# Performance work log

Measured on AMD Instinct MI355X. Metric: run time of the kernel, lower is better.

## Reference

```python
import jax, jax.numpy as jnp
import numpy as np
from jax import lax

C = 128       # capacity
D = 64        # latent_dims
K = 512       # K_vecs
BETA = 0.25
DN = ('NCHW', 'OIHW', 'NCHW')


def conv(x, w, b, stride=2, pad=1):
    y = lax.conv_general_dilated(x, w, (stride, stride), ((pad, pad), (pad, pad)),
                                 dimension_numbers=DN)
    return y + b[None, :, None, None]


def conv_transpose(x, w, b, stride=2, pad=1, k=4):
    # PyTorch ConvTranspose2d weight is (Cin, Cout, kh, kw); emulate via
    # lhs-dilated conv with spatially flipped, IO-swapped kernel.
    w2 = jnp.flip(w, axis=(-2, -1)).transpose(1, 0, 2, 3)  # -> OIHW
    p = k - 1 - pad
    y = lax.conv_general_dilated(x, w2, (1, 1), ((p, p), (p, p)),
                                 lhs_dilation=(stride, stride), dimension_numbers=DN)
    return y + b[None, :, None, None]


def setup_inputs() -> dict:
    key = jax.random.key(0)
    ks = jax.random.split(key, 11)
    s = 0.05
    return {
        'x': jax.random.uniform(ks[0], (32, 1, 256, 256), dtype=jnp.float32),
        'enc_w1': jax.random.normal(ks[1], (C, 1, 4, 4), jnp.float32) * s,
        'enc_b1': jnp.zeros((C,), jnp.float32),
        'enc_w2': jax.random.normal(ks[2], (D, C, 4, 4), jnp.float32) * s,
        'enc_b2': jnp.zeros((D,), jnp.float32),
        'codebook': jax.random.normal(ks[3], (K, D), jnp.float32),
        'dec_w2': jax.random.normal(ks[4], (D, C, 4, 4), jnp.float32) * s,  # ConvT: (Cin,Cout,kh,kw)
        'dec_b2': jnp.zeros((C,), jnp.float32),
        'dec_w1': jax.random.normal(ks[5], (C, 1, 4, 4), jnp.float32) * s,
        'dec_b1': jnp.zeros((1,), jnp.float32),
    }


def reference(x, enc_w1, enc_b1, enc_w2, enc_b2, codebook, dec_w2, dec_b2, dec_w1, dec_b1):
    # ---- encoder ----
    h = jax.nn.relu(conv(x, enc_w1, enc_b1))
    z = jax.nn.relu(conv(h, enc_w2, enc_b2))          # [B, D, H/4, W/4]

    # ---- vector quantizer ----
    z_nhwc = jnp.transpose(z, (0, 2, 3, 1))           # [B, h, w, D]
    flat = z_nhwc.reshape(-1, D)                      # [N, D]
    # mean-over-D squared distance, expanded form (no NxKxD tensor)
    d = (jnp.sum(flat * flat, axis=1, keepdims=True)
         - 2.0 * flat @ codebook.T
         + jnp.sum(codebook * codebook, axis=1)[None, :]) / D   # [N, K]
    idx = jnp.argmin(d, axis=1)                       # [N]
    quantized = codebook[idx].reshape(z_nhwc.shape)   # [B, h, w, D]

    codebook_loss = jnp.mean((quantized - lax.stop_gradient(z_nhwc)) ** 2)
    commitment_loss = jnp.mean((lax.stop_gradient(quantized) - z_nhwc) ** 2)
    vq_loss = codebook_loss + BETA * commitment_loss

    # straight-through estimator (training mode)
    quantized_st = z_nhwc + lax.stop_gradient(quantized - z_nhwc)
    q_nchw = jnp.transpose(quantized_st, (0, 3, 1, 2))

    # ---- decoder ----
    g = jax.nn.relu(conv_transpose(q_nchw, dec_w2, dec_b2))
    x_recon = jax.nn.sigmoid(conv_transpose(g, dec_w1, dec_b1))

    return vq_loss, idx[:, None].astype(jnp.int32), x_recon
```

## Files before the change

### kernel.cpp

```cpp
#include <hip/hip_runtime.h>
#include <math.h>


#define REC_OFF 131073

typedef unsigned short ushort_t;
typedef __attribute__((ext_vector_type(8))) short bf16x8;
typedef __attribute__((ext_vector_type(4))) float f32x4;
typedef __attribute__((ext_vector_type(4))) unsigned int u32x4;
union FragU { u32x4 u; bf16x8 h; };

__device__ __forceinline__ unsigned pack_hilo(float v) {
  unsigned u = __float_as_uint(v);
  unsigned htop = u & 0xFFFF0000u;
  float rf = v - __uint_as_float(htop);
  return htop | (__float_as_uint(rf) >> 16);
}
__device__ __forceinline__ ushort_t bf16_rne(float v) {
  unsigned u = __float_as_uint(v);
  u += 0x7FFFu + ((u >> 16) & 1u);
  return (ushort_t)(u >> 16);
}

__global__ __launch_bounds__(64) void zero_loss_k(float* __restrict__ out) {
  if (threadIdx.x == 0) out[0] = 0.f;
}

__global__ __launch_bounds__(256) void repackA2_k(
    const float* __restrict__ ew2,
    ushort_t* __restrict__ hi, ushort_t* __restrict__ lo) {
  int idx = blockIdx.x * 256 + threadIdx.x;
  int j = idx & 7, l = (idx >> 3) & 63, mt = (idx >> 9) & 3, ks = idx >> 11;
  int ci = ((ks >> 2) << 3) + ((l >> 4) << 1) + (j >> 2);
  int ky = ks & 3, kx = j & 3, d = (mt << 4) + (l & 15);
  float val = ew2[((d << 7) + ci) * 16 + (ky << 2) + kx];
  unsigned u = __float_as_uint(val);
  float rf = val - __uint_as_float(u & 0xFFFF0000u);
  hi[idx] = (ushort_t)(u >> 16);
  lo[idx] = (ushort_t)(__float_as_uint(rf) >> 16);
}

__global__ __launch_bounds__(256) void repackA_k(
    const float* __restrict__ dw2,
    ushort_t* __restrict__ hi, ushort_t* __restrict__ lo) {
  int idx = blockIdx.x * 256 + threadIdx.x;
  int j = idx & 7, l = (idx >> 3) & 63, mt = (idx >> 9) & 7;
  int s = (idx >> 12) & 7, v = idx >> 15;
  int co = (mt << 4) + (l & 15);
  int ci = (s << 3) + ((l >> 4) << 1) + (j >> 2);
  int tap = j & 3;
  int Yp = v >> 1, pX = v & 1;
  int kyA = 1 - Yp, kyB = kyA + 2;
  int kxA = pX ? 0 : 1, kxB = kxA + 2;
  int ky = (tap & 2) ? kyB : kyA;
  int kx = (tap & 1) ? kxA : kxB;
  float val = dw2[(((ci << 7) + co) << 4) + (ky << 2) + kx];
  unsigned u = __float_as_uint(val);
  float rf = val - __uint_as_float(u & 0xFFFF0000u);
  hi[idx] = (ushort_t)(u >> 16);
  lo[idx] = (ushort_t)(__float_as_uint(rf) >> 16);
}

__global__ __launch_bounds__(256) void repackCB_k(
    const float* __restrict__ cb,
    ushort_t* __restrict__ hi, ushort_t* __restrict__ lo) {
  int idx = blockIdx.x * 256 + threadIdx.x;
  int j = idx & 7, l = (idx >> 3) & 63, mt = (idx >> 9) & 31, ks = idx >> 14;
  int code = (mt << 4) + (l & 15);
  int k = (ks << 5) + ((l >> 4) << 3) + j;
  float val = cb[(code << 6) + k];
  unsigned u = __float_as_uint(val);
  float rf = val - __uint_as_float(u & 0xFFFF0000u);
  hi[idx] = (ushort_t)(u >> 16);
  lo[idx] = (ushort_t)(__float_as_uint(rf) >> 16);
}

__global__ __launch_bounds__(256) void csqF_k(
    const float* __restrict__ cb, float* __restrict__ csqF) {
  int idx = blockIdx.x * 256 + threadIdx.x;
  int r = idx & 3, l = (idx >> 2) & 63, mt = idx >> 8;
  int code = (mt << 4) + ((l >> 4) << 2) + r;
  const float* cp = cb + (code << 6);
  float s = 0.f;
#pragma unroll
  for (int d = 0; d < 64; ++d) s = fmaf(cp[d], cp[d], s);
  csqF[idx] = s;
}

__global__ __launch_bounds__(128) void conv1_k(
    const float* __restrict__ x, const float* __restrict__ w1,
    const float* __restrict__ b1, unsigned* __restrict__ hp) {
  int oy = blockIdx.x, b = blockIdx.y, ox = threadIdx.x;
  float xv[16];
#pragma unroll
  for (int ky = 0; ky < 4; ++ky) {
    int iy = 2 * oy - 1 + ky;
#pragma unroll
    for (int kx = 0; kx < 4; ++kx) {
      int ix = 2 * ox - 1 + kx;
      float v = 0.f;
      if (iy >= 0 && iy < 256 && ix >= 0 && ix < 256)
        v = x[(b * 256 + iy) * 256 + ix];
      xv[ky * 4 + kx] = v;
    }
  }
  for (int c = 0; c < 128; ++c) {
    const float* wp = w1 + c * 16;
    float acc = b1[c];
#pragma unroll
    for (int k = 0; k < 16; ++k) acc = fmaf(xv[k], wp[k], acc);
    hp[((b * 128 + c) * 128 + oy) * 128 + ox] = pack_hilo(fmaxf(acc, 0.f));
  }
}

#define C2RL 133
__global__ __launch_bounds__(512) void conv2_k(
    const unsigned* __restrict__ hp, const ushort_t* __restrict__ wCh,
    const ushort_t* __restrict__ wCl, const float* __restrict__ b2,
    float* __restrict__ z) {
  __shared__ unsigned hs[2][8][6][C2RL];
  int a = blockIdx.x, b = blockIdx.y;
  int t = threadIdx.x, l = t & 63;
  int w = __builtin_amdgcn_readfirstlane(t >> 6);
  int Yloc = w >> 2, mtg = (w >> 1) & 1, ntg = w & 1;
  int y = 2 * a + Yloc;
  int g = l >> 4;

  if (t < 48) {
    int ci = t & 7, r = t >> 3;
    hs[0][ci][r][0] = 0u;
    hs[0][ci][r][129] = 0u;
    hs[1][ci][r][0] = 0u;
    hs[1][ci][r][129] = 0u;
  }

  int c4 = t & 31, ci_l = (t >> 5) & 7, r0 = t >> 8;
  int yr[3];
  bool rowok[3];
#pragma unroll
  for (int i = 0; i < 3; ++i) {
    yr[i] = 4 * a - 1 + r0 + 2 * i;
    rowok[i] = yr[i] >= 0 && yr[i] < 128;
  }
  const unsigned* hbase = hp + (((long)b * 128) << 14);

  u32x4 pre[3];
#pragma unroll
  for (int i = 0; i < 3; ++i)
    pre[i] = rowok[i]
        ? *reinterpret_cast<const u32x4*>(
              hbase + (((long)ci_l << 14) + (yr[i] << 7)) + (c4 << 2))
        : (u32x4)0u;
#pragma unroll
  for (int i = 0; i < 3; ++i) {
    unsigned* dst = &hs[0][ci_l][r0 + 2 * i][1 + (c4 << 2)];
    dst[0] = pre[i][0]; dst[1] = pre[i][1];
    dst[2] = pre[i][2]; dst[3] = pre[i][3];
  }
  __syncthreads();

  f32x4 acc[2][2];
#pragma unroll
  for (int ml = 0; ml < 2; ++ml)
#pragma unroll
    for (int nl = 0; nl < 2; ++nl) acc[ml][nl] = (f32x4)0.f;

  for (int rnd = 0; rnd < 16; ++rnd) {
    int cur = rnd & 1;
    if (rnd < 15) {
      long cb8 = ((long)((rnd + 1) * 8 + ci_l)) << 14;
#pragma unroll
      for (int i = 0; i < 3; ++i)
        pre[i] = rowok[i]
            ? *reinterpret_cast<const u32x4*>(
                  hbase + cb8 + (yr[i] << 7) + (c4 << 2))
            : (u32x4)0u;
    }
#pragma unroll
    for (int ky = 0; ky < 4; ++ky) {
      int ks = (rnd << 2) + ky;
      int row = 2 * Yloc + ky;
      FragU ah[2], al_[2];
#pragma unroll
      for (int ml = 0; ml < 2; ++ml) {
        int mt = (mtg << 1) + ml;
        long aoff = (((long)ks * 4 + mt) * 64 + l) * 8;
        ah[ml].u = *reinterpret_cast<const u32x4*>(wCh + aoff);
        al_[ml].u = *reinterpret_cast<const u32x4*>(wCl + aoff);
      }
#pragma unroll
      for (int nl = 0; nl < 2; ++nl) {
        int nt = (ntg << 1) + nl;
        const unsigned* pa = &hs[cur][g * 2][row][(nt << 5) + 2 * (l & 15)];
        const unsigned* pb = &hs[cur][g * 2 + 1][row][(nt << 5) + 2 * (l & 15)];
        unsigned a0 = pa[0], a1 = pa[1], a2 = pa[2], a3 = pa[3];
        unsigned b0 = pb[0], b1 = pb[1], b2_ = pb[2], b3 = pb[3];
        FragU bh, bl;
        bh.u[0] = __builtin_amdgcn_perm(a1, a0, 0x07060302u);
        bl.u[0] = __builtin_amdgcn_perm(a1, a0, 0x05040100u);
        bh.u[1] = __builtin_amdgcn_perm(a3, a2, 0x07060302u);
        bl.u[1] = __builtin_amdgcn_perm(a3, a2, 0x05040100u);
        bh.u[2] = __builtin_amdgcn_perm(b1, b0, 0x07060302u);
        bl.u[2] = __builtin_amdgcn_perm(b1, b0, 0x05040100u);
        bh.u[3] = __builtin_amdgcn_perm(b3, b2_, 0x07060302u);
        bl.u[3] = __builtin_amdgcn_perm(b3, b2_, 0x05040100u);
#pragma unroll
        for (int ml = 0; ml < 2; ++ml) {
          acc[ml][nl] = __builtin_amdgcn_mfma_f32_16x16x32_bf16(
              ah[ml].h, bh.h, acc[ml][nl], 0, 0, 0);
          acc[ml][nl] = __builtin_amdgcn_mfma_f32_16x16x32_bf16(
              ah[ml].h, bl.h, acc[ml][nl], 0, 0, 0);
          acc[ml][nl] = __builtin_amdgcn_mfma_f32_16x16x32_bf16(
              al_[ml].h, bh.h, acc[ml][nl], 0, 0, 0);
        }
      }
    }
    if (rnd < 15) {
#pragma unroll
      for (int i = 0; i < 3; ++i) {
        unsigned* dst = &hs[cur ^ 1][ci_l][r0 + 2 * i][1 + (c4 << 2)];
        dst[0] = pre[i][0]; dst[1] = pre[i][1];
        dst[2] = pre[i][2]; dst[3] = pre[i][3];
      }
      __syncthreads();
    }
  }
#pragma unroll
  for (int ml = 0; ml < 2; ++ml) {
#pragma unroll
    for (int nl = 0; nl < 2; ++nl) {
#pragma unroll
      for (int r = 0; r < 4; ++r) {
        int d = (((mtg << 1) + ml) << 4) + (g << 2) + r;
        int x = (((ntg << 1) + nl) << 4) + (l & 15);
        float v = fmaxf(acc[ml][nl][r] + b2[d], 0.f);
        z[((b * 64 + d) * 64 + y) * 64 + x] = v;
      }
    }
  }
}

__global__ __launch_bounds__(256) void vq_k(
    const float* z, const float* __restrict__ cb,
    const ushort_t* __restrict__ cbFh, const ushort_t* __restrict__ cbFl,
    const float* __restrict__ csqF, unsigned int* q_pk,
    float* __restrict__ out, int n0) {
  __shared__ unsigned zS[64 * 67];
  __shared__ int bk_arr[64];
  __shared__ float redl[4];
  int t = threadIdx.x, l = t & 63;
  int w = __builtin_amdgcn_readfirstlane(t >> 6);
  int nbase = blockIdx.x * 64;
  int b = nbase >> 12, y = (nbase >> 6) & 63;
  long zbase = (long)b * 262144 + y * 64;

  float zv[16];
#pragma unroll
  for (int j = 0; j < 16; ++j) {
    zv[j] = z[zbase + (long)((w << 4) + j) * 4096 + l];
    zS[l * 67 + (w << 4) + j] = pack_hilo(zv[j]);
  }
  __syncthreads();

  int pp = (w << 4) + (l & 15);
  FragU bh[2], bl[2];
#pragma unroll
  for (int ks = 0; ks < 2; ++ks) {
    const unsigned* zp = &zS[pp * 67 + (ks << 5) + ((l >> 4) << 3)];
    unsigned u0 = zp[0], u1 = zp[1], u2 = zp[2], u3 = zp[3];
    unsigned u4 = zp[4], u5 = zp[5], u6 = zp[6], u7 = zp[7];
    bh[ks].u[0] = __builtin_amdgcn_perm(u1, u0, 0x07060302u);
    bl[ks].u[0] = __builtin_amdgcn_perm(u1, u0, 0x05040100u);
    bh[ks].u[1] = __builtin_amdgcn_perm(u3, u2, 0x07060302u);
    bl[ks].u[1] = __builtin_amdgcn_perm(u3, u2, 0x05040100u);
    bh[ks].u[2] = __builtin_amdgcn_perm(u5, u4, 0x07060302u);
    bl[ks].u[2] = __builtin_amdgcn_perm(u5, u4, 0x05040100u);
    bh[ks].u[3] = __builtin_amdgcn_perm(u7, u6, 0x07060302u);
    bl[ks].u[3] = __builtin_amdgcn_perm(u7, u6, 0x05040100u);
  }

  int g = l >> 4;
  float bd = 1e30f;
  int bk = 0;
  for (int mc = 0; mc < 4; ++mc) {
    f32x4 acc[8];
#pragma unroll
    for (int m8 = 0; m8 < 8; ++m8) acc[m8] = (f32x4)0.f;
#pragma unroll
    for (int ks = 0; ks < 2; ++ks) {
#pragma unroll
      for (int m8 = 0; m8 < 8; ++m8) {
        long aoff = (((long)(ks * 32 + mc * 8 + m8) * 64) + l) * 8;
        FragU ah, al_;
        ah.u = *reinterpret_cast<const u32x4*>(cbFh + aoff);
        al_.u = *reinterpret_cast<const u32x4*>(cbFl + aoff);
        acc[m8] = __builtin_amdgcn_mfma_f32_16x16x32_bf16(
            ah.h, bh[ks].h, acc[m8], 0, 0, 0);
        acc[m8] = __builtin_amdgcn_mfma_f32_16x16x32_bf16(
            ah.h, bl[ks].h, acc[m8], 0, 0, 0);
        acc[m8] = __builtin_amdgcn_mfma_f32_16x16x32_bf16(
            al_.h, bh[ks].h, acc[m8], 0, 0, 0);
      }
    }
#pragma unroll
    for (int m8 = 0; m8 < 8; ++m8) {
      int mt = mc * 8 + m8;
      f32x4 cq = *reinterpret_cast<const f32x4*>(csqF + ((mt << 6) + l) * 4);
#pragma unroll
      for (int r = 0; r < 4; ++r) {
        float d = fmaf(-2.f, acc[m8][r], cq[r]);
        if (d < bd) { bd = d; bk = (mt << 4) + (g << 2) + r; }
      }
    }
  }
#pragma unroll
  for (int m = 16; m <= 32; m <<= 1) {
    float d2 = __shfl_xor(bd, m);
    int k2 = __shfl_xor(bk, m);
    if (d2 < bd || (d2 == bd && k2 < bk)) { bd = d2; bk = k2; }
  }
  if (l < 16) {
    bk_arr[(w << 4) + l] = bk;
    out[1 + n0 + nbase + (w << 4) + l] = (float)bk;
  }
  __syncthreads();

  int bkp = bk_arr[l];
  const float* cbest = cb + (bkp << 6) + (w << 4);
  float ls = 0.f;
#pragma unroll
  for (int j = 0; j < 16; ++j) {
    float c = cbest[j];
    q_pk[zbase + (long)((w << 4) + j) * 4096 + l] = pack_hilo(c);
    float df = c - zv[j];
    ls = fmaf(df, df, ls);
  }
#pragma unroll
  for (int m = 32; m; m >>= 1) ls += __shfl_xor(ls, m);
  if (l == 0) redl[w] = ls;
  __syncthreads();
  if (t == 0)
    atomicAdd(out, (redl[0] + redl[1] + redl[2] + redl[3]) * (1.25f / 8388608.f));
}

__global__ __launch_bounds__(512) void dconv2_k(
    const unsigned int* __restrict__ q_pk, const ushort_t* __restrict__ wAh,
    const ushort_t* __restrict__ wAl, const float* __restrict__ db2,
    ushort_t* __restrict__ gp) {
  __shared__ unsigned int rows[64][3][68];
  int a = blockIdx.x, b = blockIdx.y;
  int t = threadIdx.x, l = t & 63;
  int w = __builtin_amdgcn_readfirstlane(t >> 6);
  int Yloc = w >> 2, pX = w & 1, coh = (w >> 1) & 1;
  int Y = 2 * a + Yloc;
  int v = (Yloc << 1) | pX;
  int rA = Yloc + 1, rB = Yloc;

  if (t < 192) {
    int ci = t & 63, r = t >> 6;
    rows[ci][r][0] = 0u;
    rows[ci][r][65] = 0u;
  }
  long qb = (long)b * 262144;
#pragma unroll
  for (int r = 0; r < 3; ++r) {
    int yr = a - 1 + r;
    bool ok = (yr >= 0) && (yr < 64);
    for (int s = t; s < 1024; s += 512) {
      int ci = s >> 4, c4 = s & 15;
      u32x4 val = ok ? *reinterpret_cast<const u32x4*>(
                           q_pk + qb + ci * 4096 + yr * 64 + (c4 << 2))
                     : (u32x4)0u;
      unsigned* dst = &rows[ci][r][1 + (c4 << 2)];
      dst[0] = val[0]; dst[1] = val[1]; dst[2] = val[2]; dst[3] = val[3];
    }
  }
  __syncthreads();

  f32x4 acc[4][4];
#pragma unroll
  for (int mt = 0; mt < 4; ++mt)
#pragma unroll
    for (int nt = 0; nt < 4; ++nt) acc[mt][nt] = (f32x4)0.f;

  for (int s8 = 0; s8 < 8; ++s8) {
    FragU ah[4], al[4];
#pragma unroll
    for (int mt = 0; mt < 4; ++mt) {
      long off = ((((long)(v * 8 + s8) * 8 + (coh * 4 + mt)) * 64 + l) * 8);
      ah[mt].u = *reinterpret_cast<const u32x4*>(wAh + off);
      al[mt].u = *reinterpret_cast<const u32x4*>(wAl + off);
    }
#pragma unroll
    for (int nt = 0; nt < 4; ++nt) {
      int p = nt * 16 + (l & 15) + pX;
      int cc0 = (s8 << 3) + ((l >> 4) << 1);
      unsigned u0 = rows[cc0][rA][p], u1 = rows[cc0][rA][p + 1];
      unsigned u2 = rows[cc0][rB][p], u3 = rows[cc0][rB][p + 1];
      unsigned u4 = rows[cc0 + 1][rA][p], u5 = rows[cc0 + 1][rA][p + 1];
      unsigned u6 = rows[cc0 + 1][rB][p], u7 = rows[cc0 + 1][rB][p + 1];
      FragU bh, bl;
      bh.u[0] = (u0 >> 16) | (u1 & 0xFFFF0000u);
      bl.u[0] = (u0 & 0xFFFFu) | (u1 << 16);
      bh.u[1] = (u2 >> 16) | (u3 & 0xFFFF0000u);
      bl.u[1] = (u2 & 0xFFFFu) | (u3 << 16);
      bh.u[2] = (u4 >> 16) | (u5 & 0xFFFF0000u);
      bl.u[2] = (u4 & 0xFFFFu) | (u5 << 16);
      bh.u[3] = (u6 >> 16) | (u7 & 0xFFFF0000u);
      bl.u[3] = (u6 & 0xFFFFu) | (u7 << 16);
#pragma unroll
      for (int mt = 0; mt < 4; ++mt) {
        acc[mt][nt] = __builtin_amdgcn_mfma_f32_16x16x32_bf16(
            ah[mt].h, bh.h, acc[mt][nt], 0, 0, 0);
        acc[mt][nt] = __builtin_amdgcn_mfma_f32_16x16x32_bf16(
            ah[mt].h, bl.h, acc[mt][nt], 0, 0, 0);
        acc[mt][nt] = __builtin_amdgcn_mfma_f32_16x16x32_bf16(
            al[mt].h, bh.h, acc[mt][nt], 0, 0, 0);
      }
    }
  }

#pragma unroll
  for (int mt = 0; mt < 4; ++mt) {
#pragma unroll
    for (int r = 0; r < 4; ++r) {
      int co = ((coh * 4 + mt) << 4) + ((l >> 4) << 2) + r;
      float bias = db2[co];
#pragma unroll
      for (int nt = 0; nt < 4; ++nt) {
        int X = ((nt << 4) + (l & 15)) * 2 + pX;
        float val = fmaxf(acc[mt][nt][r] + bias, 0.f);
        gp[((b * 128 + co) * 128 + Y) * 128 + X] = bf16_rne(val);
      }
    }
  }
}

__global__ __launch_bounds__(256) void dconv1_k(
    const ushort_t* __restrict__ g, const float* __restrict__ wd1,
    const float* __restrict__ db1, float* __restrict__ rec) {
  int a = blockIdx.x, b = blockIdx.y;
  int t = threadIdx.x, l = t & 63;
  int w = __builtin_amdgcn_readfirstlane(t >> 6);
  int q = 4 * a + w;
  int Y0 = 8 * a + 2 * w;
  bool ok0 = q >= 1;
  bool ok2 = q <= 126;
  const unsigned* gw = (const unsigned*)g;
  long cbase = (long)b * 128;

  float acc[8] = {0.f, 0.f, 0.f, 0.f, 0.f, 0.f, 0.f, 0.f};

  for (int ci = 0; ci < 128; ci += 2) {
    long i0 = (cbase + ci) * 128;
    long i1 = i0 + 128;
    unsigned wa[3], wb[3];
    wa[0] = ok0 ? gw[(i0 + q - 1) * 64 + l] : 0u;
    wa[1] = gw[(i0 + q) * 64 + l];
    wa[2] = ok2 ? gw[(i0 + q + 1) * 64 + l] : 0u;
    wb[0] = ok0 ? gw[(i1 + q - 1) * 64 + l] : 0u;
    wb[1] = gw[(i1 + q) * 64 + l];
    wb[2] = ok2 ? gw[(i1 + q + 1) * 64 + l] : 0u;

    const float* wp0 = wd1 + ci * 16;
    const float* wp1 = wp0 + 16;
#pragma unroll
    for (int h = 0; h < 2; ++h) {
      const unsigned* wrd = h ? wb : wa;
      const float* wp = h ? wp1 : wp0;
      float cm1[3], c0[3], c1[3], c2[3];
#pragma unroll
      for (int r = 0; r < 3; ++r) {
        unsigned wd = wrd[r];
        unsigned up = __shfl_up(wd, 1);
        unsigned dn = __shfl_down(wd, 1);
        if (l == 0) up = 0u;
        if (l == 63) dn = 0u;
        c0[r] = __uint_as_float(wd << 16);
        c1[r] = __uint_as_float(wd & 0xFFFF0000u);
        cm1[r] = __uint_as_float(up & 0xFFFF0000u);
        c2[r] = __uint_as_float(dn << 16);
      }
      acc[0] = fmaf(wp[5], c0[1], fmaf(wp[7], cm1[1],
               fmaf(wp[13], c0[0], fmaf(wp[15], cm1[0], acc[0]))));
      acc[1] = fmaf(wp[4], c1[1], fmaf(wp[6], c0[1],
               fmaf(wp[12], c1[0], fmaf(wp[14], c0[0], acc[1]))));
      acc[2] = fmaf(wp[5], c1[1], fmaf(wp[7], c0[1],
               fmaf(wp[13], c1[0], fmaf(wp[15], c0[0], acc[2]))));
      acc[3] = fmaf(wp[4], c2[1], fmaf(wp[6], c1[1],
               fmaf(wp[12], c2[0], fmaf(wp[14], c1[0], acc[3]))));
      acc[4] = fmaf(wp[1], c0[2], fmaf(wp[3], cm1[2],
               fmaf(wp[9], c0[1], fmaf(wp[11], cm1[1], acc[4]))));
      acc[5] = fmaf(wp[0], c1[2], fmaf(wp[2], c0[2],
               fmaf(wp[8], c1[1], fmaf(wp[10], c0[1], acc[5]))));
      acc[6] = fmaf(wp[1], c1[2], fmaf(wp[3], c0[2],
               fmaf(wp[9], c1[1], fmaf(wp[11], c0[1], acc[6]))));
      acc[7] = fmaf(wp[0], c2[2], fmaf(wp[2], c1[2],
               fmaf(wp[8], c2[1], fmaf(wp[10], c1[1], acc[7]))));
    }
  }
  float bb = db1[0];
  f32x4 v0, v1;
#pragma unroll
  for (int c = 0; c < 4; ++c) {
    float u = acc[c] + bb;
    v0[c] = 1.f / (1.f + __expf(-u));
    float u2 = acc[4 + c] + bb;
    v1[c] = 1.f / (1.f + __expf(-u2));
  }
  long rbase = ((long)(b * 256 + Y0)) * 256 + 4 * l;
  *reinterpret_cast<f32x4*>(&rec[rbase]) = v0;
  *reinterpret_cast<f32x4*>(&rec[rbase + 256]) = v1;
}

extern "C" void kernel_launch(void* const* d_in, const int* in_sizes, int n_in,
                              void* d_out, int out_size, void* d_ws, size_t ws_size,
                              hipStream_t stream) {
  const float* x      = (const float*)d_in[0];
  const float* enc_w1 = (const float*)d_in[1];
  const float* enc_b1 = (const float*)d_in[2];
  const float* enc_w2 = (const float*)d_in[3];
  const float* enc_b2 = (const float*)d_in[4];
  const float* cb     = (const float*)d_in[5];
  const float* dec_w2 = (const float*)d_in[6];
  const float* dec_b2 = (const float*)d_in[7];
  const float* dec_w1 = (const float*)d_in[8];
  const float* dec_b1 = (const float*)d_in[9];

  float* out = (float*)d_out;
  float* ws  = (float*)d_ws;
  ushort_t* wCh  = (ushort_t*)ws;
  ushort_t* wCl  = (ushort_t*)(ws + 65536);
  ushort_t* wAh  = (ushort_t*)(ws + 131072);
  ushort_t* wAl  = (ushort_t*)(ws + 196608);
  ushort_t* cbFh = (ushort_t*)(ws + 262144);
  ushort_t* cbFl = (ushort_t*)(ws + 278528);
  float* csqF = ws + 294912;
  float* dyn  = ws + 303104;

  const size_t PER_IMG = 2097152 + 262144;
  size_t avail = (ws_size / 4 > 303104 + 64) ? ws_size / 4 - 303104 - 64 : 0;
  int CB = 32;
  while (CB > 1 && (size_t)CB * PER_IMG > avail) CB >>= 1;

  zero_loss_k<<<dim3(1), 64, 0, stream>>>(out);
  repackA2_k<<<dim3(512), 256, 0, stream>>>(enc_w2, wCh, wCl);
  repackA_k<<<dim3(512), 256, 0, stream>>>(dec_w2, wAh, wAl);
  repackCB_k<<<dim3(128), 256, 0, stream>>>(cb, cbFh, cbFl);
  csqF_k<<<dim3(32), 256, 0, stream>>>(cb, csqF);

  for (int b0 = 0; b0 < 32; b0 += CB) {
    unsigned* hp = (unsigned*)dyn;
    float* zq = dyn + (size_t)CB * 2097152;
    conv1_k<<<dim3(128, CB), 128, 0, stream>>>(
        x + (size_t)b0 * 65536, enc_w1, enc_b1, hp);
    conv2_k<<<dim3(32, CB), 512, 0, stream>>>(hp, wCh, wCl, enc_b2, zq);
    vq_k<<<dim3(CB * 64), 256, 0, stream>>>(
        zq, cb, cbFh, cbFl, csqF, (unsigned int*)zq, out, b0 * 4096);
    dconv2_k<<<dim3(64, CB), 512, 0, stream>>>(
        (const unsigned int*)zq, wAh, wAl, dec_b2, (ushort_t*)dyn );
    dconv1_k<<<dim3(32, CB), 256, 0, stream>>>(
        (const ushort_t*)dyn , dec_w1, dec_b1,
        out + REC_OFF + (size_t)b0 * 65536);
  }
}
```

Measured before the change: 506.2 us.

## Fuse conv1 into conv2 by computing encoder hidden tiles on the fly

Removes the separate conv1 kernel and its full-resolution hidden activation buffer. Each conv2 block now loads the needed input pixels into registers and computes the ReLU'd, hi/lo-packed first-layer outputs for 8 channels per round directly into shared memory. This trades a large global write and read of the hidden tensor for redundant recomputation of halo rows, since adjacent blocks overlap by two rows. It also drops the global prefetch that overlapped loads with MFMA, so the first-layer FMAs now sit serially between MFMA rounds.

```diff
diff --git a/kernel.cpp b/kernel.cpp
--- a/kernel.cpp
+++ b/kernel.cpp
@@ -87,37 +87,35 @@
   csqF[idx] = s;
 }
 
-__global__ __launch_bounds__(128) void conv1_k(
-    const float* __restrict__ x, const float* __restrict__ w1,
-    const float* __restrict__ b1, unsigned* __restrict__ hp) {
-  int oy = blockIdx.x, b = blockIdx.y, ox = threadIdx.x;
-  float xv[16];
-#pragma unroll
-  for (int ky = 0; ky < 4; ++ky) {
-    int iy = 2 * oy - 1 + ky;
-#pragma unroll
-    for (int kx = 0; kx < 4; ++kx) {
-      int ix = 2 * ox - 1 + kx;
-      float v = 0.f;
-      if (iy >= 0 && iy < 256 && ix >= 0 && ix < 256)
-        v = x[(b * 256 + iy) * 256 + ix];
-      xv[ky * 4 + kx] = v;
-    }
-  }
-  for (int c = 0; c < 128; ++c) {
-    const float* wp = w1 + c * 16;
-    float acc = b1[c];
-#pragma unroll
-    for (int k = 0; k < 16; ++k) acc = fmaf(xv[k], wp[k], acc);
-    hp[((b * 128 + c) * 128 + oy) * 128 + ox] = pack_hilo(fmaxf(acc, 0.f));
-  }
-}
-
 #define C2RL 133
+__device__ __forceinline__ void compute_h8(
+    unsigned (*hb)[6][C2RL], int rnd, const float (&xr)[4][6],
+    int row, int p, bool vh, bool active,
+    const float* __restrict__ ew1, const float* __restrict__ eb1) {
+  if (!active) return;
+#pragma unroll
+  for (int ci = 0; ci < 8; ++ci) {
+    int c8 = (rnd << 3) + ci;
+    const float* wp = ew1 + (c8 << 4);
+    float bias = eb1[c8];
+#pragma unroll
+    for (int e = 0; e < 2; ++e) {
+      float acc = bias;
+#pragma unroll
+      for (int ky = 0; ky < 4; ++ky)
+#pragma unroll
+        for (int kx = 0; kx < 4; ++kx)
+          acc = fmaf(xr[ky][2 * e + kx], wp[ky * 4 + kx], acc);
+      hb[ci][row][1 + 2 * p + e] = vh ? pack_hilo(fmaxf(acc, 0.f)) : 0u;
+    }
+  }
+}
+
 __global__ __launch_bounds__(512) void conv2_k(
-    const unsigned* __restrict__ hp, const ushort_t* __restrict__ wCh,
-    const ushort_t* __restrict__ wCl, const float* __restrict__ b2,
-    float* __restrict__ z) {
+    const float* __restrict__ xin,
+    const float* __restrict__ ew1, const float* __restrict__ eb1,
+    const ushort_t* __restrict__ wCh, const ushort_t* __restrict__ wCl,
+    const float* __restrict__ b2, float* __restrict__ z) {
   __shared__ unsigned hs[2][8][6][C2RL];
   int a = blockIdx.x, b = blockIdx.y;
   int t = threadIdx.x, l = t & 63;
@@ -134,29 +132,31 @@
     hs[1][ci][r][129] = 0u;
   }
 
-  int c4 = t & 31, ci_l = (t >> 5) & 7, r0 = t >> 8;
-  int yr[3];
-  bool rowok[3];
-#pragma unroll
-  for (int i = 0; i < 3; ++i) {
-    yr[i] = 4 * a - 1 + r0 + 2 * i;
-    rowok[i] = yr[i] >= 0 && yr[i] < 128;
-  }
-  const unsigned* hbase = hp + (((long)b * 128) << 14);
-
-  u32x4 pre[3];
-#pragma unroll
-  for (int i = 0; i < 3; ++i)
-    pre[i] = rowok[i]
-        ? *reinterpret_cast<const u32x4*>(
-              hbase + (((long)ci_l << 14) + (yr[i] << 7)) + (c4 << 2))
-        : (u32x4)0u;
-#pragma unroll
-  for (int i = 0; i < 3; ++i) {
-    unsigned* dst = &hs[0][ci_l][r0 + 2 * i][1 + (c4 << 2)];
-    dst[0] = pre[i][0]; dst[1] = pre[i][1];
-    dst[2] = pre[i][2]; dst[3] = pre[i][3];
-  }
+  int row = t >> 6, p = t & 63;
+  bool hactive = row < 6;
+  int hy = 4 * a - 1 + row;
+  bool vh = hy >= 0 && hy < 128;
+  const float* xb = xin + ((long)b << 16);
+  float xr[4][6];
+#pragma unroll
+  for (int r = 0; r < 4; ++r)
+#pragma unroll
+    for (int c = 0; c < 6; ++c) xr[r][c] = 0.f;
+  if (hactive) {
+#pragma unroll
+    for (int r = 0; r < 4; ++r) {
+      int gy = 8 * a - 3 + 2 * row + r;
+      bool oky = gy >= 0 && gy < 256;
+#pragma unroll
+      for (int c = 0; c < 6; ++c) {
+        int gx = 4 * p - 1 + c;
+        bool okx = gx >= 0 && gx < 256;
+        xr[r][c] = (oky && okx) ? xb[(gy << 8) + gx] : 0.f;
+      }
+    }
+  }
+
+  compute_h8(hs[0], 0, xr, row, p, vh, hactive, ew1, eb1);
   __syncthreads();
 
   f32x4 acc[2][2];
@@ -167,19 +167,10 @@
 
   for (int rnd = 0; rnd < 16; ++rnd) {
     int cur = rnd & 1;
-    if (rnd < 15) {
-      long cb8 = ((long)((rnd + 1) * 8 + ci_l)) << 14;
-#pragma unroll
-      for (int i = 0; i < 3; ++i)
-        pre[i] = rowok[i]
-            ? *reinterpret_cast<const u32x4*>(
-                  hbase + cb8 + (yr[i] << 7) + (c4 << 2))
-            : (u32x4)0u;
-    }
 #pragma unroll
     for (int ky = 0; ky < 4; ++ky) {
       int ks = (rnd << 2) + ky;
-      int row = 2 * Yloc + ky;
+      int lrow = 2 * Yloc + ky;
       FragU ah[2], al_[2];
 #pragma unroll
       for (int ml = 0; ml < 2; ++ml) {
@@ -191,8 +182,8 @@
 #pragma unroll
       for (int nl = 0; nl < 2; ++nl) {
         int nt = (ntg << 1) + nl;
-        const unsigned* pa = &hs[cur][g * 2][row][(nt << 5) + 2 * (l & 15)];
-        const unsigned* pb = &hs[cur][g * 2 + 1][row][(nt << 5) + 2 * (l & 15)];
+        const unsigned* pa = &hs[cur][g * 2][lrow][(nt << 5) + 2 * (l & 15)];
+        const unsigned* pb = &hs[cur][g * 2 + 1][lrow][(nt << 5) + 2 * (l & 15)];
         unsigned a0 = pa[0], a1 = pa[1], a2 = pa[2], a3 = pa[3];
         unsigned b0 = pb[0], b1 = pb[1], b2_ = pb[2], b3 = pb[3];
         FragU bh, bl;
@@ -216,12 +207,7 @@
       }
     }
     if (rnd < 15) {
-#pragma unroll
-      for (int i = 0; i < 3; ++i) {
-        unsigned* dst = &hs[cur ^ 1][ci_l][r0 + 2 * i][1 + (c4 << 2)];
-        dst[0] = pre[i][0]; dst[1] = pre[i][1];
-        dst[2] = pre[i][2]; dst[3] = pre[i][3];
-      }
+      compute_h8(hs[cur ^ 1], rnd + 1, xr, row, p, vh, hactive, ew1, eb1);
       __syncthreads();
     }
   }
@@ -550,11 +536,9 @@
   csqF_k<<<dim3(32), 256, 0, stream>>>(cb, csqF);
 
   for (int b0 = 0; b0 < 32; b0 += CB) {
-    unsigned* hp = (unsigned*)dyn;
     float* zq = dyn + (size_t)CB * 2097152;
-    conv1_k<<<dim3(128, CB), 128, 0, stream>>>(
-        x + (size_t)b0 * 65536, enc_w1, enc_b1, hp);
-    conv2_k<<<dim3(32, CB), 512, 0, stream>>>(hp, wCh, wCl, enc_b2, zq);
+    conv2_k<<<dim3(32, CB), 512, 0, stream>>>(
+        x + (size_t)b0 * 65536, enc_w1, enc_b1, wCh, wCl, enc_b2, zq);
     vq_k<<<dim3(CB * 64), 256, 0, stream>>>(
         zq, cb, cbFh, cbFl, csqF, (unsigned int*)zq, out, b0 * 4096);
     dconv2_k<<<dim3(64, CB), 512, 0, stream>>>(
```

Measured after the change: 490.7 us, median of 2. 1.03x faster.
